# Kernel tuning notes

Hardware: AMD Instinct MI355X
Metric: run time of the kernel (lower is better)

## Reference

```python
import jax, jax.numpy as jnp
import numpy as np
from jax import lax

MIN_DELTA = 0.5 / 2 ** 3  # COMPATIBLE = False path
MAX_STEP = 20
MAX_CAMSTEP = 6
# (name, n_options, action_range_start) for non-camera discrete actions.
# range_start follows the original: commit=[0,1], camera=[1,6], then cumulative n-1.
ACTS = [("forward_back", 3, 6), ("left_right", 3, 8), ("jump", 2, 10),
        ("sneak_sprint", 4, 11), ("attack", 32, 14)]
N_ACTIONS = 45  # 6 + sum(n-1) = 6 + 39


def _forward(fc_input, camera, acts, W1, b1, W2, b2):
    B = fc_input.shape[0]
    dt = fc_input.dtype
    cam0, cam1 = camera[:, 0], camera[:, 1]
    acts = {k: v.astype(jnp.int32) for k, v in acts.items()}

    def step(carry, _):
        ac, delta, chosen, rdac, cam_steps, commited = carry
        alive = ~commited  # loss mask for this step (norm accounting in original)
        # build fc0 extra input: [current_ac(2), one-hots(44), delta(1), delta_chosen(1)]
        parts = [ac]
        for name, n, lo in ACTS:
            parts.append(jax.nn.one_hot(rdac[name], n, dtype=dt))
        step_in = jnp.concatenate(parts + [delta[:, None], chosen.astype(dt)[:, None]], axis=1)

        # ---- target dac computation (torch.no_grad block) ----
        commit = ((jnp.abs(cam0) < 1e-5) & (jnp.abs(cam1) < 1e-5)) | (cam_steps >= MAX_CAMSTEP)
        for name, n, lo in ACTS:
            commit = commit & (rdac[name] == acts[name])
        dac = jnp.zeros((B,), jnp.int32)
        modified = commit
        new_rdac = {}
        for name, n, lo in ACTS:
            a = acts[name]
            r = rdac[name]
            disc = (~modified) & (r != a)
            val = jnp.where(a == 0, r - 1 + lo, a - 1 + lo).astype(jnp.int32)
            dac = jnp.where(disc, val, dac)
            new_rdac[name] = jnp.where(disc, a, r)
            modified = modified | disc
        ac0, ac1 = ac[:, 0], ac[:, 1]
        # NOTE: original compares both camera components against ac[:, 0] (faithful).
        delta_mask = (~modified) & (~chosen) & (
            (jnp.abs(cam0 - ac0) > delta * 2.0) | (jnp.abs(cam1 - ac0) > delta * 2.0))
        dac = jnp.where(delta_mask, 5, dac)
        delta = jnp.where(delta_mask, jnp.clip(delta * 2.0, -0.5, 0.5), delta)
        modified = modified | delta_mask
        m = ~modified
        incX = cam0 >= ac0
        incY = cam1 >= ac1
        # quadrants: decX&decY->1, incX&decY->2, decX&incY->3, incX&incY->4
        dac = jnp.where(m, 1 + incX.astype(jnp.int32) + 2 * incY.astype(jnp.int32), dac)
        sx = jnp.where(incX, delta, -delta)
        sy = jnp.where(incY, delta, -delta)
        ac = jnp.stack([jnp.where(m, ac0 + sx, ac0), jnp.where(m, ac1 + sy, ac1)], axis=1)
        delta = jnp.where(m, delta * 0.5, delta)
        chosen = chosen | m
        cam_steps = cam_steps + m.astype(jnp.int32)
        commited = commited | commit
        return (ac, delta, chosen, new_rdac, cam_steps, commited), (step_in, dac, alive)

    init = (jnp.zeros((B, 2), dt),
            jnp.full((B,), MIN_DELTA, dt),
            jnp.zeros((B,), bool),
            {name: jnp.zeros((B,), jnp.int32) for name, _, _ in ACTS},
            jnp.zeros((B,), jnp.int32),
            jnp.zeros((B,), bool))
    _, (step_ins, dacs, alives) = lax.scan(step, init, None, length=MAX_STEP)
    # step_ins: [T,B,48], dacs: [T,B], alives: [T,B]
    T = MAX_STEP
    x = jnp.concatenate(
        [jnp.broadcast_to(fc_input[None], (T,) + fc_input.shape), step_ins], axis=-1)
    x = x.reshape(T * B, -1)
    h = x @ W1 + b1
    h = h * jax.nn.sigmoid(h)  # swish
    logits = h @ W2 + b2
    logp = jax.nn.log_softmax(logits, axis=-1)
    ce = -jnp.take_along_axis(logp, dacs.reshape(-1, 1), axis=1)[:, 0].reshape(T, B)
    af = alives.astype(ce.dtype)
    loss = (ce * af).sum(0) / af.sum(0)  # per-sample loss normalized by #active steps
    return loss.mean()


def setup_inputs() -> dict:
    key = jax.random.key(0)
    ks = jax.random.split(key, 10)
    B, NI, H = 4096, 1024, 2048
    D_IN = NI + 4 + 44  # 1072
    return {
        "fc_input": jax.random.normal(ks[0], (B, NI), jnp.float32),
        "camera": jax.random.normal(ks[1], (B, 2), jnp.float32),
        "forward_back": jax.random.randint(ks[2], (B,), 0, 3),
        "left_right": jax.random.randint(ks[3], (B,), 0, 3),
        "jump": jax.random.randint(ks[4], (B,), 0, 2),
        "sneak_sprint": jax.random.randint(ks[5], (B,), 0, 4),
        "attack": jax.random.randint(ks[6], (B,), 0, 32),
        "W1": jax.random.normal(ks[7], (D_IN, H), jnp.float32) * 0.02,
        "b1": jnp.zeros((H,), jnp.float32),
        "W2": jax.random.normal(ks[8], (H, N_ACTIONS), jnp.float32) * 0.02,
        "b2": jnp.zeros((N_ACTIONS,), jnp.float32),
    }


def reference(fc_input, camera, forward_back, left_right, jump, sneak_sprint, attack,
              W1, b1, W2, b2):
    acts = {"forward_back": forward_back, "left_right": left_right, "jump": jump,
            "sneak_sprint": sneak_sprint, "attack": attack}
    return _forward(fc_input, camera, acts, W1, b1, W2, b2)
```

## Files before the change

### kernel.cpp

```cpp
#include <hip/hip_runtime.h>

#define BATCH 4096
#define NI 1024
#define HID 2048
#define TSTEPS 20
#define NA 45
#define TW 512
#define SROW 520
#define MAXS 16
#define NB 2

typedef __bf16 bf16x8 __attribute__((ext_vector_type(8)));
typedef float floatx4 __attribute__((ext_vector_type(4)));

struct StepMeta {
    float ac0, ac1, delta, chosen;
    int chg;
    int dac, mult, pad;
};

__device__ __forceinline__ unsigned short f2bf(float x) {
    union { float f; unsigned int u; } un; un.f = x;
    unsigned int r = un.u + 0x7FFFu + ((un.u >> 16) & 1u);
    return (unsigned short)(r >> 16);
}

__device__ void scan_one(int b, const float* __restrict__ camera,
                         const int* __restrict__ fb_in, const int* __restrict__ lr_in,
                         const int* __restrict__ jp_in, const int* __restrict__ ss_in,
                         const int* __restrict__ at_in, StepMeta* __restrict__ meta,
                         int2* __restrict__ hdr) {
    float cam0 = camera[2 * b], cam1 = camera[2 * b + 1];
    int afb = fb_in[b], alr = lr_in[b], ajp = jp_in[b], ass = ss_in[b], aat = at_in[b];
    float ac0 = 0.f, ac1 = 0.f, delta = 0.0625f;
    int rfb = 0, rlr = 0, rjp = 0, rss = 0, rat = 0;
    bool chosen = false;
    int cam_steps = 0;
    int chgPending = -1;
    bool camzero = (fabsf(cam0) < 1e-5f) && (fabsf(cam1) < 1e-5f);
    int nd = 0, aliveTot = 0;
    float lac0 = 0.f, lac1 = 0.f, ldelta = 0.f, lchosen = 0.f;
    int ldac = -1000;
    for (int t = 0; t < TSTEPS; t++) {
        StepMeta m;
        m.ac0 = ac0; m.ac1 = ac1; m.delta = delta; m.chosen = chosen ? 1.f : 0.f;
        m.chg = chgPending; chgPending = -1;
        bool commit = (camzero || cam_steps >= 6) &&
                      rfb == afb && rlr == alr && rjp == ajp && rss == ass && rat == aat;
        int dac = 0; bool modified = commit;
        if (!modified && rfb != afb) { dac = (afb == 0 ? rfb - 1 + 6  : afb - 1 + 6 ); chgPending = ((2  + rfb) << 8) | (2  + afb); rfb = afb; modified = true; }
        if (!modified && rlr != alr) { dac = (alr == 0 ? rlr - 1 + 8  : alr - 1 + 8 ); chgPending = ((5  + rlr) << 8) | (5  + alr); rlr = alr; modified = true; }
        if (!modified && rjp != ajp) { dac = (ajp == 0 ? rjp - 1 + 10 : ajp - 1 + 10); chgPending = ((8  + rjp) << 8) | (8  + ajp); rjp = ajp; modified = true; }
        if (!modified && rss != ass) { dac = (ass == 0 ? rss - 1 + 11 : ass - 1 + 11); chgPending = ((10 + rss) << 8) | (10 + ass); rss = ass; modified = true; }
        if (!modified && rat != aat) { dac = (aat == 0 ? rat - 1 + 14 : aat - 1 + 14); chgPending = ((14 + rat) << 8) | (14 + aat); rat = aat; modified = true; }
        if (!modified && !chosen &&
            (fabsf(cam0 - ac0) > delta * 2.f || fabsf(cam1 - ac0) > delta * 2.f)) {
            dac = 5; delta = fminf(delta * 2.f, 0.5f); modified = true;
        }
        if (!modified) {
            bool incX = cam0 >= ac0, incY = cam1 >= ac1;
            dac = 1 + (incX ? 1 : 0) + (incY ? 2 : 0);
            ac0 += incX ? delta : -delta;
            ac1 += incY ? delta : -delta;
            delta *= 0.5f;
            chosen = true;
            cam_steps++;
        }
        m.dac = dac; m.mult = 1; m.pad = 0;
        if (nd > 0 && m.chg < 0 && !commit &&
            m.ac0 == lac0 && m.ac1 == lac1 && m.delta == ldelta &&
            m.chosen == lchosen && dac == ldac) {
            meta[b * MAXS + nd - 1].mult = 1 + (TSTEPS - t);
            aliveTot += (TSTEPS - t);
            break;
        }
        meta[b * MAXS + nd] = m;
        lac0 = m.ac0; lac1 = m.ac1; ldelta = m.delta; lchosen = m.chosen; ldac = dac;
        nd++; aliveTot++;
        if (commit) break;
    }
    hdr[b] = make_int2(nd, aliveTot);
}

__global__ void prep_kernel(const float* __restrict__ fc, unsigned short* __restrict__ Ab,
                            const float* __restrict__ W1, unsigned short* __restrict__ Wt,
                            const float* __restrict__ W2, unsigned short* __restrict__ W2T,
                            const float* __restrict__ camera,
                            const int* __restrict__ fb_in, const int* __restrict__ lr_in,
                            const int* __restrict__ jp_in, const int* __restrict__ ss_in,
                            const int* __restrict__ at_in, StepMeta* __restrict__ meta,
                            int2* __restrict__ hdr) {
    __shared__ float tile[32][33];
    int bid = blockIdx.x, tid = threadIdx.x;
    if (bid < 4096) {
        int idx = bid * 256 + tid;
        float4 v = ((const float4*)fc)[idx];
        ushort4 o;
        o.x = f2bf(v.x); o.y = f2bf(v.y); o.z = f2bf(v.z); o.w = f2bf(v.w);
        ((ushort4*)Ab)[idx] = o;
    } else if (bid < 6144) {
        int b2 = bid - 4096;
        int k0 = (b2 & 31) * 32, n0 = (b2 >> 5) * 32;
        int tx = tid & 31, ty = tid >> 5;
        for (int i = 0; i < 4; i++)
            tile[ty + 8 * i][tx] = W1[(size_t)(k0 + ty + 8 * i) * HID + n0 + tx];
        __syncthreads();
        for (int i = 0; i < 4; i++) {
            int n = ty + 8 * i;
            Wt[(size_t)(n0 + n) * NI + k0 + tx] = f2bf(tile[tx][n]);
        }
    } else if (bid < 6152) {
        int k = (bid - 6144) * 256 + tid;
        for (int n = 0; n < 48; n++)
            W2T[(size_t)n * HID + k] = (n < NA) ? f2bf(W2[(size_t)k * NA + n]) : (unsigned short)0;
    } else {
        int b = (bid - 6152) * 256 + tid;
        scan_one(b, camera, fb_in, lr_in, jp_in, ss_in, at_in, meta, hdr);
    }
}

__global__ __launch_bounds__(512) void gemm_base(const unsigned short* __restrict__ Ab,
                                                 const unsigned short* __restrict__ Wt,
                                                 const float* __restrict__ W1,
                                                 const float* __restrict__ b1,
                                                 float* __restrict__ C) {
    __shared__ __align__(16) __bf16 At[128 * 32];
    __shared__ __align__(16) __bf16 Bt[128 * 32];
    int bn = blockIdx.x, bm = blockIdx.y;
    int m0 = bm * 128, n0 = bn * 128;
    int tid = threadIdx.x;
    int wave = tid >> 6, lane = tid & 63;
    int wr = wave >> 2, wc = wave & 3;
    int l15 = lane & 15, q = lane >> 4;
    floatx4 acc[4][2];
    for (int a = 0; a < 4; a++) for (int c = 0; c < 2; c++) acc[a][c] = (floatx4){0.f, 0.f, 0.f, 0.f};
    for (int k0 = 0; k0 < NI; k0 += 32) {
        __syncthreads();
        {
            int c = tid;
            int row = c >> 2, quarter = c & 3;
            const unsigned short* gA = &Ab[(size_t)(m0 + row) * NI + k0 + quarter * 8];
            const unsigned short* gB = &Wt[(size_t)(n0 + row) * NI + k0 + quarter * 8];
            __builtin_amdgcn_global_load_lds(
                (const __attribute__((address_space(1))) unsigned int*)gA,
                (__attribute__((address_space(3))) unsigned int*)&At[c * 8], 16, 0, 0);
            __builtin_amdgcn_global_load_lds(
                (const __attribute__((address_space(1))) unsigned int*)gB,
                (__attribute__((address_space(3))) unsigned int*)&Bt[c * 8], 16, 0, 0);
        }
        __syncthreads();
        bf16x8 af[4], bf[2];
        for (int mr = 0; mr < 4; mr++)
            af[mr] = *(const bf16x8*)&At[(wr * 64 + mr * 16 + l15) * 32 + q * 8];
        for (int nc = 0; nc < 2; nc++)
            bf[nc] = *(const bf16x8*)&Bt[(wc * 32 + nc * 16 + l15) * 32 + q * 8];
        for (int mr = 0; mr < 4; mr++)
            for (int nc = 0; nc < 2; nc++)
                acc[mr][nc] = __builtin_amdgcn_mfma_f32_16x16x32_bf16(af[mr], bf[nc], acc[mr][nc], 0, 0, 0);
    }
    for (int nc = 0; nc < 2; nc++) {
        int col = n0 + wc * 32 + nc * 16 + l15;
        const float* We = W1 + (size_t)NI * HID + col;
        float cv = b1[col] + We[2 * HID] + We[5 * HID] + We[8 * HID] + We[10 * HID]
                 + We[14 * HID] + 0.0625f * We[46 * HID];
        for (int mr = 0; mr < 4; mr++)
            for (int r = 0; r < 4; r++) {
                int row = m0 + wr * 64 + mr * 16 + q * 4 + r;
                C[(size_t)row * HID + col] = acc[mr][nc][r] + cv;
            }
    }
}

__global__ __launch_bounds__(512, 4) void fused_mlp(const float* __restrict__ base,
                                                 const float* __restrict__ W1,
                                                 const unsigned short* __restrict__ W2T,
                                                 const float* __restrict__ b2,
                                                 const StepMeta* __restrict__ meta,
                                                 const int2* __restrict__ hdr,
                                                 float* __restrict__ loss_out) {
    __shared__ __align__(16) __bf16 S[NB * MAXS * SROW];
    __shared__ __align__(16) float4 u4s[NB][MAXS];
    __shared__ int chgs[NB][MAXS], dacsS[NB][MAXS], multsS[NB][MAXS];
    __shared__ int swapL[NB][5], nsS[NB], ndS[NB], atS[NB];
    __shared__ float b2s[48];
    __shared__ float ceArr[NB][MAXS];
    __shared__ float pmax[NB][MAXS][12], psum[NB][MAXS][12], mxS[NB][MAXS];

    int bp = blockIdx.x, tid = threadIdx.x;
    int tg = tid >> 8, tl = tid & 255;
    int wave = tid >> 6, lane = tid & 63, l15 = lane & 15, q = lane >> 4;

    if (tl == 0) {
        int2 hd = hdr[bp * NB + tg];
        ndS[tg] = hd.x; atS[tg] = hd.y;
    }
    if (tl < MAXS) {
        StepMeta m = meta[(size_t)(bp * NB + tg) * MAXS + tl];
        u4s[tg][tl] = make_float4(m.ac0, m.ac1, m.delta - 0.0625f, m.chosen);
        chgs[tg][tl] = m.chg; dacsS[tg][tl] = m.dac; multsS[tg][tl] = m.mult;
    }
    if (tid >= 64 && tid < 112) {
        int n = tid - 64;
        b2s[n] = (n < NA) ? b2[n] : 0.f;
    }
    __syncthreads();
    if (tl == 0) {
        int ns = 0, nd = ndS[tg];
        for (int s = 0; s < nd; s++)
            if (chgs[tg][s] >= 0) swapL[tg][ns++] = chgs[tg][s];
        nsS[tg] = ns;
        for (; ns < 5; ns++) swapL[tg][ns] = 0;
    }
    __syncthreads();

    const float* Wx = W1 + (size_t)NI * HID;
    const __bf16* Wb = (const __bf16*)W2T;
    floatx4 acc[2][3];
    for (int a = 0; a < 2; a++) for (int c = 0; c < 3; c++) acc[a][c] = (floatx4){0.f, 0.f, 0.f, 0.f};

    int nd = __builtin_amdgcn_readfirstlane(ndS[tg]);
    int ns = __builtin_amdgcn_readfirstlane(nsS[tg]);
    int cA = __builtin_amdgcn_readfirstlane(swapL[tg][0]);
    int cB = __builtin_amdgcn_readfirstlane(swapL[tg][1]);
    int cC = __builtin_amdgcn_readfirstlane(swapL[tg][2]);
    int cD = __builtin_amdgcn_readfirstlane(swapL[tg][3]);
    int cE = __builtin_amdgcn_readfirstlane(swapL[tg][4]);

    for (int jt = 0; jt < 4; jt++) {
        if (jt) __syncthreads();
        bf16x8 wb[2][3];
#pragma unroll
        for (int i = 0; i < 2; i++) {
            int kg = jt * TW + (wave + 8 * i) * 32 + q * 8;
            wb[i][0] = *(const bf16x8*)&Wb[(size_t)l15 * HID + kg];
            wb[i][1] = *(const bf16x8*)&Wb[(size_t)(16 + l15) * HID + kg];
            wb[i][2] = *(const bf16x8*)&Wb[(size_t)(32 + l15) * HID + kg];
        }
        int j = jt * TW + 2 * tl;
        float2 w0  = *(const float2*)&Wx[j];
        float2 w1  = *(const float2*)&Wx[HID + j];
        float2 wdl = *(const float2*)&Wx[46 * HID + j];
        float2 wch = *(const float2*)&Wx[47 * HID + j];
        float2 hb  = *(const float2*)&base[(size_t)(bp * NB + tg) * HID + j];
        float2 nA = {0,0}, oA = {0,0}, nB = {0,0}, oB = {0,0}, nC = {0,0}, oC = {0,0};
        float2 nD = {0,0}, oD = {0,0}, nE = {0,0}, oE = {0,0};
        if (ns > 0) { nA = *(const float2*)&Wx[(size_t)(cA & 255) * HID + j]; oA = *(const float2*)&Wx[(size_t)(cA >> 8) * HID + j]; }
        if (ns > 1) { nB = *(const float2*)&Wx[(size_t)(cB & 255) * HID + j]; oB = *(const float2*)&Wx[(size_t)(cB >> 8) * HID + j]; }
        if (ns > 2) { nC = *(const float2*)&Wx[(size_t)(cC & 255) * HID + j]; oC = *(const float2*)&Wx[(size_t)(cC >> 8) * HID + j]; }
        if (ns > 3) { nD = *(const float2*)&Wx[(size_t)(cD & 255) * HID + j]; oD = *(const float2*)&Wx[(size_t)(cD >> 8) * HID + j]; }
        if (ns > 4) { nE = *(const float2*)&Wx[(size_t)(cE & 255) * HID + j]; oE = *(const float2*)&Wx[(size_t)(cE >> 8) * HID + j]; }

        auto compute1 = [&](int s, float bx, float by) {
            float4 u = u4s[tg][s];
            float t0 = fmaf(u.x, w0.x, bx);
            float m0 = u.y * w1.x;  m0 = fmaf(u.z, wdl.x, m0);
            t0 = fmaf(u.w, wch.x, t0);
            float h0 = t0 + m0;
            float t1 = fmaf(u.x, w0.y, by);
            float m1 = u.y * w1.y;  m1 = fmaf(u.z, wdl.y, m1);
            t1 = fmaf(u.w, wch.y, t1);
            float h1 = t1 + m1;
            float s0 = h0 * __builtin_amdgcn_rcpf(1.f + __expf(-h0));
            float s1 = h1 * __builtin_amdgcn_rcpf(1.f + __expf(-h1));
            union { unsigned int u32; __bf16 h[2]; } pk;
            pk.h[0] = (__bf16)s0; pk.h[1] = (__bf16)s1;
            *(unsigned int*)&S[(size_t)(tg * MAXS + s) * SROW + 2 * tl] = pk.u32;
        };

        float swx = 0.f, swy = 0.f;
        compute1(0, hb.x, hb.y);
        if (ns > 0) { swx += nA.x - oA.x; swy += nA.y - oA.y; compute1(1, hb.x + swx, hb.y + swy); }
        if (ns > 1) { swx += nB.x - oB.x; swy += nB.y - oB.y; compute1(2, hb.x + swx, hb.y + swy); }
        if (ns > 2) { swx += nC.x - oC.x; swy += nC.y - oC.y; compute1(3, hb.x + swx, hb.y + swy); }
        if (ns > 3) { swx += nD.x - oD.x; swy += nD.y - oD.y; compute1(4, hb.x + swx, hb.y + swy); }
        if (ns > 4) { swx += nE.x - oE.x; swy += nE.y - oE.y; compute1(5, hb.x + swx, hb.y + swy); }
        float bx = hb.x + swx, by = hb.y + swy;
        int s = ns + 1;
        for (; s + 1 < nd; s += 2) {
            compute1(s, bx, by);
            compute1(s + 1, bx, by);
        }
        if (s < nd) compute1(s, bx, by);

        __syncthreads();
#pragma unroll
        for (int i = 0; i < 2; i++) {
            int kc = (wave + 8 * i) * 32 + q * 8;
            bf16x8 a0 = *(const bf16x8*)&S[(size_t)l15 * SROW + kc];
            bf16x8 a1 = *(const bf16x8*)&S[(size_t)(MAXS + l15) * SROW + kc];
            acc[0][0] = __builtin_amdgcn_mfma_f32_16x16x32_bf16(a0, wb[i][0], acc[0][0], 0, 0, 0);
            acc[0][1] = __builtin_amdgcn_mfma_f32_16x16x32_bf16(a0, wb[i][1], acc[0][1], 0, 0, 0);
            acc[0][2] = __builtin_amdgcn_mfma_f32_16x16x32_bf16(a0, wb[i][2], acc[0][2], 0, 0, 0);
            acc[1][0] = __builtin_amdgcn_mfma_f32_16x16x32_bf16(a1, wb[i][0], acc[1][0], 0, 0, 0);
            acc[1][1] = __builtin_amdgcn_mfma_f32_16x16x32_bf16(a1, wb[i][1], acc[1][1], 0, 0, 0);
            acc[1][2] = __builtin_amdgcn_mfma_f32_16x16x32_bf16(a1, wb[i][2], acc[1][2], 0, 0, 0);
        }
    }
    __syncthreads();
    float* logitsP = (float*)S;
    float* logitsF = (float*)S + 6144;
    if (wave >= 4) {
        int wv = wave - 4;
#pragma unroll
        for (int mt = 0; mt < 2; mt++)
#pragma unroll
            for (int nt = 0; nt < 3; nt++)
#pragma unroll
                for (int r = 0; r < 4; r++)
                    logitsP[(size_t)(wv * 2 + mt) * 768 + (q * 4 + r) * 48 + nt * 16 + l15] = acc[mt][nt][r];
    }
    __syncthreads();
    if (wave < 4) {
        int wv = wave;
#pragma unroll
        for (int mt = 0; mt < 2; mt++)
#pragma unroll
            for (int nt = 0; nt < 3; nt++)
#pragma unroll
                for (int r = 0; r < 4; r++) {
                    size_t idx = (size_t)(wv * 2 + mt) * 768 + (q * 4 + r) * 48 + nt * 16 + l15;
                    logitsP[idx] += acc[mt][nt][r];
                }
    }
    __syncthreads();
    int tg2 = tid / 192, tl2 = tid - tg2 * 192;
    int tE = tl2 / 12, gE = tl2 - tE * 12;
    if (tid < 384) {
        const float4* P0 = (const float4*)(logitsP + (size_t)(0 * 2 + tg2) * 768);
        const float4* P1 = (const float4*)(logitsP + (size_t)(1 * 2 + tg2) * 768);
        const float4* P2 = (const float4*)(logitsP + (size_t)(2 * 2 + tg2) * 768);
        const float4* P3 = (const float4*)(logitsP + (size_t)(3 * 2 + tg2) * 768);
        float4 p0 = P0[tl2], p1 = P1[tl2], p2 = P2[tl2], p3 = P3[tl2];
        float4 bb = *(const float4*)&b2s[gE * 4];
        float4 r;
        r.x = p0.x + p1.x + p2.x + p3.x + bb.x;
        r.y = p0.y + p1.y + p2.y + p3.y + bb.y;
        r.z = p0.z + p1.z + p2.z + p3.z + bb.z;
        r.w = p0.w + p1.w + p2.w + p3.w + bb.w;
        ((float4*)(logitsF + tg2 * 768))[tl2] = r;
        float lm = (gE == 11) ? r.x : fmaxf(fmaxf(r.x, r.y), fmaxf(r.z, r.w));
        pmax[tg2][tE][gE] = lm;
    }
    __syncthreads();
    if (tid < 384 && gE == 0) {
        float m = pmax[tg2][tE][0];
        for (int i = 1; i < 12; i++) m = fmaxf(m, pmax[tg2][tE][i]);
        mxS[tg2][tE] = m;
    }
    __syncthreads();
    if (tid < 384) {
        float m = mxS[tg2][tE];
        float4 v = ((const float4*)(logitsF + tg2 * 768))[tl2];
        float s;
        if (gE == 11) s = __expf(v.x - m);
        else s = __expf(v.x - m) + __expf(v.y - m) + __expf(v.z - m) + __expf(v.w - m);
        psum[tg2][tE][gE] = s;
    }
    __syncthreads();
    if (tl < nd) {
        float ssum = 0.f;
        for (int i = 0; i < 12; i++) ssum += psum[tg][tl][i];
        float m = mxS[tg][tl];
        int dac = dacsS[tg][tl];
        float ld = logitsF[tg * 768 + tl * 48 + dac];
        float ce = -(ld - m - logf(ssum));
        ceArr[tg][tl] = ce * (float)multsS[tg][tl];
    }
    __syncthreads();
    if (tl == 0) {
        float s = 0.f;
        for (int t = 0; t < nd; t++) s += ceArr[tg][t];
        loss_out[bp * NB + tg] = s / (float)atS[tg];
    }
}

__global__ void reduce_loss(const float* __restrict__ loss, float* __restrict__ out) {
    int tid = threadIdx.x;
    float s = 0.f;
    for (int i = tid; i < BATCH; i += 256) s += loss[i];
    for (int off = 32; off > 0; off >>= 1) s += __shfl_down(s, off, 64);
    __shared__ float wsum[4];
    if ((tid & 63) == 0) wsum[tid >> 6] = s;
    __syncthreads();
    if (tid == 0) out[0] = (wsum[0] + wsum[1] + wsum[2] + wsum[3]) * (1.0f / (float)BATCH);
}

extern "C" void kernel_launch(void* const* d_in, const int* in_sizes, int n_in,
                              void* d_out, int out_size, void* d_ws, size_t ws_size,
                              hipStream_t stream) {
    const float* fc_input = (const float*)d_in[0];
    const float* camera   = (const float*)d_in[1];
    const int*   fb       = (const int*)d_in[2];
    const int*   lr       = (const int*)d_in[3];
    const int*   jp       = (const int*)d_in[4];
    const int*   ss       = (const int*)d_in[5];
    const int*   at       = (const int*)d_in[6];
    const float* W1       = (const float*)d_in[7];
    const float* b1       = (const float*)d_in[8];
    const float* W2       = (const float*)d_in[9];
    const float* b2       = (const float*)d_in[10];
    float* out = (float*)d_out;

    char* ws = (char*)d_ws;
    unsigned short* Ab   = (unsigned short*)(ws);
    unsigned short* Wt   = (unsigned short*)(ws + 8388608);
    float*          baseB= (float*)(ws + 12582912);
    StepMeta*       meta = (StepMeta*)(ws + 46137344);
    int2*           hdr  = (int2*)(ws + 48234496);
    float*          lossB= (float*)(ws + 48267264);
    unsigned short* W2T  = (unsigned short*)(ws + 48283648);

    prep_kernel<<<4096 + 2048 + 8 + 16, 256, 0, stream>>>(fc_input, Ab, W1, Wt, W2, W2T,
                                                          camera, fb, lr, jp, ss, at, meta, hdr);
    gemm_base<<<dim3(HID / 128, BATCH / 128), 512, 0, stream>>>(Ab, Wt, W1, b1, baseB);
    fused_mlp<<<BATCH / NB, 512, 0, stream>>>(baseB, W1, W2T, b2, meta, hdr, lossB);
    reduce_loss<<<1, 256, 0, stream>>>(lossB, out);
}
```

Before: 223.0 us.

## Balance hidden-row work across block halves and parallelize W2 transpose

In the fused MLP kernel, the two 256-thread halves no longer each own one batch sample. They now split the combined set of distinct step rows of both samples evenly, so a sample with many steps no longer leaves the other half idle. W2T operand loads move from before the elementwise phase to just before the MFMAs, which cuts live registers, and swap deltas are precomputed as differences. The W2 transpose in prep now runs over 128 blocks instead of 8 strided loops. In exchange every thread loads both samples' base rows and swap weights, which adds redundant global loads and branching.

```diff
diff --git a/kernel.cpp b/kernel.cpp
--- a/kernel.cpp
+++ b/kernel.cpp
@@ -109,12 +109,17 @@
             int n = ty + 8 * i;
             Wt[(size_t)(n0 + n) * NI + k0 + tx] = f2bf(tile[tx][n]);
         }
-    } else if (bid < 6152) {
-        int k = (bid - 6144) * 256 + tid;
-        for (int n = 0; n < 48; n++)
+    } else if (bid < 6272) {
+        int bid2 = bid - 6144;
+        int k = bid2 * 16 + (tid >> 4);
+        int nn = tid & 15;
+#pragma unroll
+        for (int i = 0; i < 3; i++) {
+            int n = nn * 3 + i;
             W2T[(size_t)n * HID + k] = (n < NA) ? f2bf(W2[(size_t)k * NA + n]) : (unsigned short)0;
+        }
     } else {
-        int b = (bid - 6152) * 256 + tid;
+        int b = (bid - 6272) * 256 + tid;
         scan_one(b, camera, fb_in, lr_in, jp_in, ss_in, at_in, meta, hdr);
     }
 }
@@ -188,6 +193,7 @@
 
     int bp = blockIdx.x, tid = threadIdx.x;
     int tg = tid >> 8, tl = tid & 255;
+    int c = tid & 255, half = tid >> 8;
     int wave = tid >> 6, lane = tid & 63, l15 = lane & 15, q = lane >> 4;
 
     if (tl == 0) {
@@ -216,42 +222,50 @@
     const float* Wx = W1 + (size_t)NI * HID;
     const __bf16* Wb = (const __bf16*)W2T;
     floatx4 acc[2][3];
-    for (int a = 0; a < 2; a++) for (int c = 0; c < 3; c++) acc[a][c] = (floatx4){0.f, 0.f, 0.f, 0.f};
-
-    int nd = __builtin_amdgcn_readfirstlane(ndS[tg]);
-    int ns = __builtin_amdgcn_readfirstlane(nsS[tg]);
-    int cA = __builtin_amdgcn_readfirstlane(swapL[tg][0]);
-    int cB = __builtin_amdgcn_readfirstlane(swapL[tg][1]);
-    int cC = __builtin_amdgcn_readfirstlane(swapL[tg][2]);
-    int cD = __builtin_amdgcn_readfirstlane(swapL[tg][3]);
-    int cE = __builtin_amdgcn_readfirstlane(swapL[tg][4]);
+    for (int a = 0; a < 2; a++) for (int cc = 0; cc < 3; cc++) acc[a][cc] = (floatx4){0.f, 0.f, 0.f, 0.f};
+
+    int nd0 = __builtin_amdgcn_readfirstlane(ndS[0]);
+    int nd1 = __builtin_amdgcn_readfirstlane(ndS[1]);
+    int ns0 = __builtin_amdgcn_readfirstlane(nsS[0]);
+    int ns1 = __builtin_amdgcn_readfirstlane(nsS[1]);
+    int cA0 = __builtin_amdgcn_readfirstlane(swapL[0][0]);
+    int cB0 = __builtin_amdgcn_readfirstlane(swapL[0][1]);
+    int cC0 = __builtin_amdgcn_readfirstlane(swapL[0][2]);
+    int cD0 = __builtin_amdgcn_readfirstlane(swapL[0][3]);
+    int cE0 = __builtin_amdgcn_readfirstlane(swapL[0][4]);
+    int cA1 = __builtin_amdgcn_readfirstlane(swapL[1][0]);
+    int cB1 = __builtin_amdgcn_readfirstlane(swapL[1][1]);
+    int cC1 = __builtin_amdgcn_readfirstlane(swapL[1][2]);
+    int cD1 = __builtin_amdgcn_readfirstlane(swapL[1][3]);
+    int cE1 = __builtin_amdgcn_readfirstlane(swapL[1][4]);
+    int U = nd0 + nd1, hcut = (U + 1) >> 1;
+    int kb = half ? hcut : 0;
+    int ke = half ? U : hcut;
 
     for (int jt = 0; jt < 4; jt++) {
         if (jt) __syncthreads();
-        bf16x8 wb[2][3];
-#pragma unroll
-        for (int i = 0; i < 2; i++) {
-            int kg = jt * TW + (wave + 8 * i) * 32 + q * 8;
-            wb[i][0] = *(const bf16x8*)&Wb[(size_t)l15 * HID + kg];
-            wb[i][1] = *(const bf16x8*)&Wb[(size_t)(16 + l15) * HID + kg];
-            wb[i][2] = *(const bf16x8*)&Wb[(size_t)(32 + l15) * HID + kg];
-        }
-        int j = jt * TW + 2 * tl;
+        int j = jt * TW + 2 * c;
         float2 w0  = *(const float2*)&Wx[j];
         float2 w1  = *(const float2*)&Wx[HID + j];
         float2 wdl = *(const float2*)&Wx[46 * HID + j];
         float2 wch = *(const float2*)&Wx[47 * HID + j];
-        float2 hb  = *(const float2*)&base[(size_t)(bp * NB + tg) * HID + j];
-        float2 nA = {0,0}, oA = {0,0}, nB = {0,0}, oB = {0,0}, nC = {0,0}, oC = {0,0};
-        float2 nD = {0,0}, oD = {0,0}, nE = {0,0}, oE = {0,0};
-        if (ns > 0) { nA = *(const float2*)&Wx[(size_t)(cA & 255) * HID + j]; oA = *(const float2*)&Wx[(size_t)(cA >> 8) * HID + j]; }
-        if (ns > 1) { nB = *(const float2*)&Wx[(size_t)(cB & 255) * HID + j]; oB = *(const float2*)&Wx[(size_t)(cB >> 8) * HID + j]; }
-        if (ns > 2) { nC = *(const float2*)&Wx[(size_t)(cC & 255) * HID + j]; oC = *(const float2*)&Wx[(size_t)(cC >> 8) * HID + j]; }
-        if (ns > 3) { nD = *(const float2*)&Wx[(size_t)(cD & 255) * HID + j]; oD = *(const float2*)&Wx[(size_t)(cD >> 8) * HID + j]; }
-        if (ns > 4) { nE = *(const float2*)&Wx[(size_t)(cE & 255) * HID + j]; oE = *(const float2*)&Wx[(size_t)(cE >> 8) * HID + j]; }
-
-        auto compute1 = [&](int s, float bx, float by) {
-            float4 u = u4s[tg][s];
+        float2 hb0 = *(const float2*)&base[(size_t)(bp * NB + 0) * HID + j];
+        float2 hb1 = *(const float2*)&base[(size_t)(bp * NB + 1) * HID + j];
+        float dA0x=0,dA0y=0,dB0x=0,dB0y=0,dC0x=0,dC0y=0,dD0x=0,dD0y=0,dE0x=0,dE0y=0;
+        float dA1x=0,dA1y=0,dB1x=0,dB1y=0,dC1x=0,dC1y=0,dD1x=0,dD1y=0,dE1x=0,dE1y=0;
+        if (ns0 > 0) { float2 n_ = *(const float2*)&Wx[(size_t)(cA0 & 255) * HID + j], o_ = *(const float2*)&Wx[(size_t)(cA0 >> 8) * HID + j]; dA0x = n_.x - o_.x; dA0y = n_.y - o_.y; }
+        if (ns0 > 1) { float2 n_ = *(const float2*)&Wx[(size_t)(cB0 & 255) * HID + j], o_ = *(const float2*)&Wx[(size_t)(cB0 >> 8) * HID + j]; dB0x = n_.x - o_.x; dB0y = n_.y - o_.y; }
+        if (ns0 > 2) { float2 n_ = *(const float2*)&Wx[(size_t)(cC0 & 255) * HID + j], o_ = *(const float2*)&Wx[(size_t)(cC0 >> 8) * HID + j]; dC0x = n_.x - o_.x; dC0y = n_.y - o_.y; }
+        if (ns0 > 3) { float2 n_ = *(const float2*)&Wx[(size_t)(cD0 & 255) * HID + j], o_ = *(const float2*)&Wx[(size_t)(cD0 >> 8) * HID + j]; dD0x = n_.x - o_.x; dD0y = n_.y - o_.y; }
+        if (ns0 > 4) { float2 n_ = *(const float2*)&Wx[(size_t)(cE0 & 255) * HID + j], o_ = *(const float2*)&Wx[(size_t)(cE0 >> 8) * HID + j]; dE0x = n_.x - o_.x; dE0y = n_.y - o_.y; }
+        if (ns1 > 0) { float2 n_ = *(const float2*)&Wx[(size_t)(cA1 & 255) * HID + j], o_ = *(const float2*)&Wx[(size_t)(cA1 >> 8) * HID + j]; dA1x = n_.x - o_.x; dA1y = n_.y - o_.y; }
+        if (ns1 > 1) { float2 n_ = *(const float2*)&Wx[(size_t)(cB1 & 255) * HID + j], o_ = *(const float2*)&Wx[(size_t)(cB1 >> 8) * HID + j]; dB1x = n_.x - o_.x; dB1y = n_.y - o_.y; }
+        if (ns1 > 2) { float2 n_ = *(const float2*)&Wx[(size_t)(cC1 & 255) * HID + j], o_ = *(const float2*)&Wx[(size_t)(cC1 >> 8) * HID + j]; dC1x = n_.x - o_.x; dC1y = n_.y - o_.y; }
+        if (ns1 > 3) { float2 n_ = *(const float2*)&Wx[(size_t)(cD1 & 255) * HID + j], o_ = *(const float2*)&Wx[(size_t)(cD1 >> 8) * HID + j]; dD1x = n_.x - o_.x; dD1y = n_.y - o_.y; }
+        if (ns1 > 4) { float2 n_ = *(const float2*)&Wx[(size_t)(cE1 & 255) * HID + j], o_ = *(const float2*)&Wx[(size_t)(cE1 >> 8) * HID + j]; dE1x = n_.x - o_.x; dE1y = n_.y - o_.y; }
+
+        auto compute1 = [&](int row, float bx, float by) {
+            float4 u = ((const float4*)u4s)[row];
             float t0 = fmaf(u.x, w0.x, bx);
             float m0 = u.y * w1.x;  m0 = fmaf(u.z, wdl.x, m0);
             t0 = fmaf(u.w, wch.x, t0);
@@ -264,23 +278,37 @@
             float s1 = h1 * __builtin_amdgcn_rcpf(1.f + __expf(-h1));
             union { unsigned int u32; __bf16 h[2]; } pk;
             pk.h[0] = (__bf16)s0; pk.h[1] = (__bf16)s1;
-            *(unsigned int*)&S[(size_t)(tg * MAXS + s) * SROW + 2 * tl] = pk.u32;
+            *(unsigned int*)&S[(size_t)row * SROW + 2 * c] = pk.u32;
         };
 
-        float swx = 0.f, swy = 0.f;
-        compute1(0, hb.x, hb.y);
-        if (ns > 0) { swx += nA.x - oA.x; swy += nA.y - oA.y; compute1(1, hb.x + swx, hb.y + swy); }
-        if (ns > 1) { swx += nB.x - oB.x; swy += nB.y - oB.y; compute1(2, hb.x + swx, hb.y + swy); }
-        if (ns > 2) { swx += nC.x - oC.x; swy += nC.y - oC.y; compute1(3, hb.x + swx, hb.y + swy); }
-        if (ns > 3) { swx += nD.x - oD.x; swy += nD.y - oD.y; compute1(4, hb.x + swx, hb.y + swy); }
-        if (ns > 4) { swx += nE.x - oE.x; swy += nE.y - oE.y; compute1(5, hb.x + swx, hb.y + swy); }
-        float bx = hb.x + swx, by = hb.y + swy;
-        int s = ns + 1;
-        for (; s + 1 < nd; s += 2) {
-            compute1(s, bx, by);
-            compute1(s + 1, bx, by);
-        }
-        if (s < nd) compute1(s, bx, by);
+        {
+            float swx = 0.f, swy = 0.f;
+            if (kb == 0) compute1(0, hb0.x, hb0.y);
+            if (ns0 > 0) { swx += dA0x; swy += dA0y; if (1 >= kb && 1 < ke) compute1(1, hb0.x + swx, hb0.y + swy); }
+            if (ns0 > 1) { swx += dB0x; swy += dB0y; if (2 >= kb && 2 < ke) compute1(2, hb0.x + swx, hb0.y + swy); }
+            if (ns0 > 2) { swx += dC0x; swy += dC0y; if (3 >= kb && 3 < ke) compute1(3, hb0.x + swx, hb0.y + swy); }
+            if (ns0 > 3) { swx += dD0x; swy += dD0y; if (4 >= kb && 4 < ke) compute1(4, hb0.x + swx, hb0.y + swy); }
+            if (ns0 > 4) { swx += dE0x; swy += dE0y; if (5 >= kb && 5 < ke) compute1(5, hb0.x + swx, hb0.y + swy); }
+            float bx = hb0.x + swx, by = hb0.y + swy;
+            int s_lo = max(ns0 + 1, kb), s_hi = min(nd0, ke);
+            int s = s_lo;
+            for (; s + 1 < s_hi; s += 2) { compute1(s, bx, by); compute1(s + 1, bx, by); }
+            if (s < s_hi) compute1(s, bx, by);
+        }
+        {
+            float swx = 0.f, swy = 0.f;
+            if (nd0 >= kb && nd0 < ke) compute1(MAXS + 0, hb1.x, hb1.y);
+            if (ns1 > 0) { swx += dA1x; swy += dA1y; if (nd0 + 1 >= kb && nd0 + 1 < ke) compute1(MAXS + 1, hb1.x + swx, hb1.y + swy); }
+            if (ns1 > 1) { swx += dB1x; swy += dB1y; if (nd0 + 2 >= kb && nd0 + 2 < ke) compute1(MAXS + 2, hb1.x + swx, hb1.y + swy); }
+            if (ns1 > 2) { swx += dC1x; swy += dC1y; if (nd0 + 3 >= kb && nd0 + 3 < ke) compute1(MAXS + 3, hb1.x + swx, hb1.y + swy); }
+            if (ns1 > 3) { swx += dD1x; swy += dD1y; if (nd0 + 4 >= kb && nd0 + 4 < ke) compute1(MAXS + 4, hb1.x + swx, hb1.y + swy); }
+            if (ns1 > 4) { swx += dE1x; swy += dE1y; if (nd0 + 5 >= kb && nd0 + 5 < ke) compute1(MAXS + 5, hb1.x + swx, hb1.y + swy); }
+            float bx = hb1.x + swx, by = hb1.y + swy;
+            int s_lo = max(ns1 + 1, kb - nd0), s_hi = min(nd1, ke - nd0);
+            int s = s_lo;
+            for (; s + 1 < s_hi; s += 2) { compute1(MAXS + s, bx, by); compute1(MAXS + s + 1, bx, by); }
+            if (s < s_hi) compute1(MAXS + s, bx, by);
+        }
 
         __syncthreads();
 #pragma unroll
@@ -288,12 +316,16 @@
             int kc = (wave + 8 * i) * 32 + q * 8;
             bf16x8 a0 = *(const bf16x8*)&S[(size_t)l15 * SROW + kc];
             bf16x8 a1 = *(const bf16x8*)&S[(size_t)(MAXS + l15) * SROW + kc];
-            acc[0][0] = __builtin_amdgcn_mfma_f32_16x16x32_bf16(a0, wb[i][0], acc[0][0], 0, 0, 0);
-            acc[0][1] = __builtin_amdgcn_mfma_f32_16x16x32_bf16(a0, wb[i][1], acc[0][1], 0, 0, 0);
-            acc[0][2] = __builtin_amdgcn_mfma_f32_16x16x32_bf16(a0, wb[i][2], acc[0][2], 0, 0, 0);
-            acc[1][0] = __builtin_amdgcn_mfma_f32_16x16x32_bf16(a1, wb[i][0], acc[1][0], 0, 0, 0);
-            acc[1][1] = __builtin_amdgcn_mfma_f32_16x16x32_bf16(a1, wb[i][1], acc[1][1], 0, 0, 0);
-            acc[1][2] = __builtin_amdgcn_mfma_f32_16x16x32_bf16(a1, wb[i][2], acc[1][2], 0, 0, 0);
+            int kg = jt * TW + kc;
+            bf16x8 b0  = *(const bf16x8*)&Wb[(size_t)l15 * HID + kg];
+            bf16x8 b1v = *(const bf16x8*)&Wb[(size_t)(16 + l15) * HID + kg];
+            bf16x8 b2v = *(const bf16x8*)&Wb[(size_t)(32 + l15) * HID + kg];
+            acc[0][0] = __builtin_amdgcn_mfma_f32_16x16x32_bf16(a0, b0,  acc[0][0], 0, 0, 0);
+            acc[0][1] = __builtin_amdgcn_mfma_f32_16x16x32_bf16(a0, b1v, acc[0][1], 0, 0, 0);
+            acc[0][2] = __builtin_amdgcn_mfma_f32_16x16x32_bf16(a0, b2v, acc[0][2], 0, 0, 0);
+            acc[1][0] = __builtin_amdgcn_mfma_f32_16x16x32_bf16(a1, b0,  acc[1][0], 0, 0, 0);
+            acc[1][1] = __builtin_amdgcn_mfma_f32_16x16x32_bf16(a1, b1v, acc[1][1], 0, 0, 0);
+            acc[1][2] = __builtin_amdgcn_mfma_f32_16x16x32_bf16(a1, b2v, acc[1][2], 0, 0, 0);
         }
     }
     __syncthreads();
@@ -357,19 +389,23 @@
         psum[tg2][tE][gE] = s;
     }
     __syncthreads();
-    if (tl < nd) {
-        float ssum = 0.f;
-        for (int i = 0; i < 12; i++) ssum += psum[tg][tl][i];
-        float m = mxS[tg][tl];
-        int dac = dacsS[tg][tl];
-        float ld = logitsF[tg * 768 + tl * 48 + dac];
-        float ce = -(ld - m - logf(ssum));
-        ceArr[tg][tl] = ce * (float)multsS[tg][tl];
+    {
+        int ndE = __builtin_amdgcn_readfirstlane(ndS[tg]);
+        if (tl < ndE) {
+            float ssum = 0.f;
+            for (int i = 0; i < 12; i++) ssum += psum[tg][tl][i];
+            float m = mxS[tg][tl];
+            int dac = dacsS[tg][tl];
+            float ld = logitsF[tg * 768 + tl * 48 + dac];
+            float ce = -(ld - m - logf(ssum));
+            ceArr[tg][tl] = ce * (float)multsS[tg][tl];
+        }
     }
     __syncthreads();
     if (tl == 0) {
+        int ndE = ndS[tg];
         float s = 0.f;
-        for (int t = 0; t < nd; t++) s += ceArr[tg][t];
+        for (int t = 0; t < ndE; t++) s += ceArr[tg][t];
         loss_out[bp * NB + tg] = s / (float)atS[tg];
     }
 }
@@ -410,8 +446,8 @@
     float*          lossB= (float*)(ws + 48267264);
     unsigned short* W2T  = (unsigned short*)(ws + 48283648);
 
-    prep_kernel<<<4096 + 2048 + 8 + 16, 256, 0, stream>>>(fc_input, Ab, W1, Wt, W2, W2T,
-                                                          camera, fb, lr, jp, ss, at, meta, hdr);
+    prep_kernel<<<4096 + 2048 + 128 + 16, 256, 0, stream>>>(fc_input, Ab, W1, Wt, W2, W2T,
+                                                            camera, fb, lr, jp, ss, at, meta, hdr);
     gemm_base<<<dim3(HID / 128, BATCH / 128), 512, 0, stream>>>(Ab, Wt, W1, b1, baseB);
     fused_mlp<<<BATCH / NB, 512, 0, stream>>>(baseB, W1, W2T, b2, meta, hdr, lossB);
     reduce_loss<<<1, 256, 0, stream>>>(lossB, out);
```

After: 250.0 us. +12.1%, slower.
